# Optimization experiments

Measured on AMD Instinct MI355X. Metric: run time of the kernel, lower is better.

Reference implementation:

```python
import jax, jax.numpy as jnp
import numpy as np


def setup_inputs() -> dict:
    key = jax.random.key(0)
    k1, k2, k3, k4 = jax.random.split(key, 4)
    B, S, D_IN, D_OUT = 32, 4096, 256, 256
    input = jax.random.normal(k1, (B, S, D_IN), dtype=jnp.float32)
    data_mask = jax.random.randint(k2, (B, S), 0, 2).astype(jnp.bool_)
    W = jax.random.normal(k3, (D_IN, D_OUT), dtype=jnp.float32) * (1.0 / np.sqrt(D_IN))
    b = jax.random.normal(k4, (D_OUT,), dtype=jnp.float32) * 0.01
    return {"input": input, "data_mask": data_mask, "W": W, "b": b}


def reference(input, data_mask, W, b):
    # ObjWise: gather non-pad tokens, apply op (Linear+ReLU), scatter back,
    # pad positions filled with zeros. Since the op is per-token, this equals
    # applying the op everywhere and zeroing pad positions.
    # input: (B, S, D_in), data_mask: (B, S)
    y = jax.nn.relu(jnp.einsum("bsd,de->bse", input, W) + b)  # (B, S, D_out)
    return jnp.where(data_mask[..., None], y, jnp.zeros((), dtype=y.dtype))
```

## Files before the change

### kernel.cpp

```cpp
#include <hip/hip_runtime.h>
#include <hip/hip_bf16.h>


typedef __attribute__((ext_vector_type(8))) short bf16x8;
typedef __attribute__((ext_vector_type(4))) float f32x4;
typedef __attribute__((ext_vector_type(2))) unsigned int u32x2;

#define KD 256
#define ND 256
#define BM 64

static __device__ __forceinline__ unsigned short f2bf(float f) {
  union { float f; unsigned u; } x; x.f = f;
  unsigned r = x.u + 0x7FFFu + ((x.u >> 16) & 1u);
  return (unsigned short)(r >> 16);
}

static __device__ __forceinline__ bool mrow(const void* mp, int flag, size_t row) {
  if (flag == 2) return ((const float*)mp)[row] != 0.0f;
  if (flag == 1) return ((const unsigned char*)mp)[row] != 0;
  return ((const int*)mp)[row] != 0;
}

__global__ void prep_w_kernel(const float* __restrict__ W,
                              unsigned short* __restrict__ wf,
                              const unsigned int* __restrict__ mw,
                              int* __restrict__ flag) {
  int k = blockIdx.x;
  int n = threadIdx.x;
  float v = W[k * ND + n];
  int nb = n >> 4;
  int kb = k >> 5;
  int lane = (n & 15) | (((k >> 3) & 3) << 4);
  int e = k & 7;
  wf[(((nb << 3) | kb) << 9) + (lane << 3) + e] = f2bf(v);

  if (blockIdx.x == 0) {
    __shared__ int s;
    if (threadIdx.x == 0) s = 0;
    __syncthreads();
    unsigned w = mw[threadIdx.x];
    int f = 0;
    if (w == 0x3F800000u) f = 2;
    else if (w > 1u) f = 1;
    if (f) atomicOr(&s, f);
    __syncthreads();
    if (threadIdx.x == 0) *flag = (s & 2) ? 2 : (s & 1);
  }
}

__global__ __launch_bounds__(256, 4) void objwise_gemm(
    const float* __restrict__ A, const void* __restrict__ mask,
    const unsigned short* __restrict__ wf, const float* __restrict__ bias,
    float* __restrict__ out, const int* __restrict__ flagp) {
  __shared__ __align__(16) unsigned char As[BM * KD * 2];

  const int flag = *flagp;
  const int tid  = threadIdx.x;
  const int wave = tid >> 6;
  const int lane = tid & 63;
  const size_t rowbase = (size_t)blockIdx.x * BM;

  const float* Ab = A + rowbase * KD;
#pragma unroll
  for (int i = 0; i < 16; ++i) {
    f32x4 v = *(const f32x4*)(Ab + i * 1024 + tid * 4);
    int row  = (i << 2) + (tid >> 6);
    int colb = (tid << 3) & 511;
    int baddr = ((row << 9) | colb) ^ ((row & 7) << 4);
    unsigned p0 = (unsigned)f2bf(v[0]) | ((unsigned)f2bf(v[1]) << 16);
    unsigned p1 = (unsigned)f2bf(v[2]) | ((unsigned)f2bf(v[3]) << 16);
    *(u32x2*)(As + baddr) = (u32x2){p0, p1};
  }
  __syncthreads();

  const int cb = wave << 6;
  const unsigned short* wfl = wf + ((size_t)(cb >> 4) << 12) + (lane << 3);

  f32x4 acc[4][4];
#pragma unroll
  for (int fr = 0; fr < 4; ++fr)
#pragma unroll
    for (int nb = 0; nb < 4; ++nb)
      acc[fr][nb] = (f32x4){0.f, 0.f, 0.f, 0.f};

  const int arow_l = lane & 15;
  const int gbyte  = (lane >> 4) << 4;

#pragma unroll 2
  for (int kb = 0; kb < 8; ++kb) {
    bf16x8 af[4];
#pragma unroll
    for (int fr = 0; fr < 4; ++fr) {
      int row  = (fr << 4) + arow_l;
      int addr = (((row << 9) | ((kb << 6) + gbyte))) ^ ((row & 7) << 4);
      af[fr] = *(const bf16x8*)(As + addr);
    }
#pragma unroll
    for (int nb = 0; nb < 4; ++nb) {
      bf16x8 bfr = *(const bf16x8*)(wfl + ((size_t)nb << 12) + (kb << 9));
      acc[0][nb] = __builtin_amdgcn_mfma_f32_16x16x32_bf16(af[0], bfr, acc[0][nb], 0, 0, 0);
      acc[1][nb] = __builtin_amdgcn_mfma_f32_16x16x32_bf16(af[1], bfr, acc[1][nb], 0, 0, 0);
      acc[2][nb] = __builtin_amdgcn_mfma_f32_16x16x32_bf16(af[2], bfr, acc[2][nb], 0, 0, 0);
      acc[3][nb] = __builtin_amdgcn_mfma_f32_16x16x32_bf16(af[3], bfr, acc[3][nb], 0, 0, 0);
    }
  }

  const int col0 = cb + (lane & 15);
  float bvs[4];
#pragma unroll
  for (int nb = 0; nb < 4; ++nb) bvs[nb] = bias[col0 + (nb << 4)];

#pragma unroll
  for (int fr = 0; fr < 4; ++fr) {
    const int rl = (fr << 4) + ((lane >> 4) << 2);
#pragma unroll
    for (int j = 0; j < 4; ++j) {
      const size_t grow = rowbase + rl + j;
      const bool mm = mrow(mask, flag, grow);
      float* op = out + grow * ND + col0;
#pragma unroll
      for (int nb = 0; nb < 4; ++nb) {
        float v = fmaxf(acc[fr][nb][j] + bvs[nb], 0.f);
        op[nb << 4] = mm ? v : 0.f;
      }
    }
  }
}

extern "C" void kernel_launch(void* const* d_in, const int* in_sizes, int n_in,
                              void* d_out, int out_size, void* d_ws, size_t ws_size,
                              hipStream_t stream) {
  const float* A    = (const float*)d_in[0];
  const void*  mask = d_in[1];
  const float* W    = (const float*)d_in[2];
  const float* bias = (const float*)d_in[3];
  float* out = (float*)d_out;

  int* flag = (int*)d_ws;
  unsigned short* wf = (unsigned short*)((char*)d_ws + 256);

  prep_w_kernel<<<256, 256, 0, stream>>>(W, wf, (const unsigned int*)mask, flag);
  objwise_gemm<<<2048, 256, 0, stream>>>(A, mask, wf, bias, out, flag);
}
```

Baseline: 258.6 us.

## Persist blocks over 4 tiles, prefetch next tile, skip loads of masked rows

Each block now handles four consecutive 64-row tiles. The next tile's fp32 input is loaded into registers while the current tile runs its MFMA loop, and the LDS buffer is double-buffered. A wave ballot over the mask lets the kernel skip global loads for padded rows, which cuts input read traffic by about half, and the mask bits are reused in the epilogue. The risks are extra register pressure from the prefetch registers (launch bounds drop to 2 blocks per CU) and a smaller grid.

```diff
diff --git a/kernel.cpp b/kernel.cpp
--- a/kernel.cpp
+++ b/kernel.cpp
@@ -9,6 +9,8 @@
 #define KD 256
 #define ND 256
 #define BM 64
+#define TILES 4
+#define GRID 512
 
 static __device__ __forceinline__ unsigned short f2bf(float f) {
   union { float f; unsigned u; } x; x.f = f;
@@ -49,82 +51,111 @@
   }
 }
 
-__global__ __launch_bounds__(256, 4) void objwise_gemm(
+__global__ __launch_bounds__(256, 2) void objwise_gemm(
     const float* __restrict__ A, const void* __restrict__ mask,
     const unsigned short* __restrict__ wf, const float* __restrict__ bias,
     float* __restrict__ out, const int* __restrict__ flagp) {
-  __shared__ __align__(16) unsigned char As[BM * KD * 2];
+  __shared__ __align__(16) unsigned char As[2][BM * KD * 2];
 
   const int flag = *flagp;
   const int tid  = threadIdx.x;
   const int wave = tid >> 6;
   const int lane = tid & 63;
-  const size_t rowbase = (size_t)blockIdx.x * BM;
+  const int tile0 = blockIdx.x * TILES;
 
-  const float* Ab = A + rowbase * KD;
-#pragma unroll
-  for (int i = 0; i < 16; ++i) {
-    f32x4 v = *(const f32x4*)(Ab + i * 1024 + tid * 4);
-    int row  = (i << 2) + (tid >> 6);
-    int colb = (tid << 3) & 511;
-    int baddr = ((row << 9) | colb) ^ ((row & 7) << 4);
-    unsigned p0 = (unsigned)f2bf(v[0]) | ((unsigned)f2bf(v[1]) << 16);
-    unsigned p1 = (unsigned)f2bf(v[2]) | ((unsigned)f2bf(v[3]) << 16);
-    *(u32x2*)(As + baddr) = (u32x2){p0, p1};
-  }
-  __syncthreads();
+  const int srowL = tid >> 6;
+  const int colb  = (tid << 3) & 511;
 
   const int cb = wave << 6;
   const unsigned short* wfl = wf + ((size_t)(cb >> 4) << 12) + (lane << 3);
 
-  f32x4 acc[4][4];
-#pragma unroll
-  for (int fr = 0; fr < 4; ++fr)
-#pragma unroll
-    for (int nb = 0; nb < 4; ++nb)
-      acc[fr][nb] = (f32x4){0.f, 0.f, 0.f, 0.f};
-
   const int arow_l = lane & 15;
   const int gbyte  = (lane >> 4) << 4;
-
-#pragma unroll 2
-  for (int kb = 0; kb < 8; ++kb) {
-    bf16x8 af[4];
-#pragma unroll
-    for (int fr = 0; fr < 4; ++fr) {
-      int row  = (fr << 4) + arow_l;
-      int addr = (((row << 9) | ((kb << 6) + gbyte))) ^ ((row & 7) << 4);
-      af[fr] = *(const bf16x8*)(As + addr);
-    }
-#pragma unroll
-    for (int nb = 0; nb < 4; ++nb) {
-      bf16x8 bfr = *(const bf16x8*)(wfl + ((size_t)nb << 12) + (kb << 9));
-      acc[0][nb] = __builtin_amdgcn_mfma_f32_16x16x32_bf16(af[0], bfr, acc[0][nb], 0, 0, 0);
-      acc[1][nb] = __builtin_amdgcn_mfma_f32_16x16x32_bf16(af[1], bfr, acc[1][nb], 0, 0, 0);
-      acc[2][nb] = __builtin_amdgcn_mfma_f32_16x16x32_bf16(af[2], bfr, acc[2][nb], 0, 0, 0);
-      acc[3][nb] = __builtin_amdgcn_mfma_f32_16x16x32_bf16(af[3], bfr, acc[3][nb], 0, 0, 0);
-    }
-  }
-
-  const int col0 = cb + (lane & 15);
+  const int col0   = cb + (lane & 15);
   float bvs[4];
 #pragma unroll
   for (int nb = 0; nb < 4; ++nb) bvs[nb] = bias[col0 + (nb << 4)];
 
+  f32x4 pre[16];
 #pragma unroll
-  for (int fr = 0; fr < 4; ++fr) {
-    const int rl = (fr << 4) + ((lane >> 4) << 2);
+  for (int i = 0; i < 16; ++i) pre[i] = (f32x4){0.f, 0.f, 0.f, 0.f};
+
+  unsigned long long bm = __ballot(mrow(mask, flag, (size_t)tile0 * BM + lane));
+  {
+    const float* Ab = A + (size_t)tile0 * BM * KD;
 #pragma unroll
-    for (int j = 0; j < 4; ++j) {
-      const size_t grow = rowbase + rl + j;
-      const bool mm = mrow(mask, flag, grow);
-      float* op = out + grow * ND + col0;
+    for (int i = 0; i < 16; ++i) {
+      int rowL = (i << 2) + srowL;
+      if ((bm >> rowL) & 1ULL) pre[i] = *(const f32x4*)(Ab + i * 1024 + tid * 4);
+    }
+  }
+
+  for (int t = 0; t < TILES; ++t) {
+    const size_t rowbase = (size_t)(tile0 + t) * BM;
+    unsigned char* Al = As[t & 1];
+
+#pragma unroll
+    for (int i = 0; i < 16; ++i) {
+      int row   = (i << 2) + srowL;
+      int baddr = ((row << 9) | colb) ^ ((row & 7) << 4);
+      unsigned p0 = (unsigned)f2bf(pre[i][0]) | ((unsigned)f2bf(pre[i][1]) << 16);
+      unsigned p1 = (unsigned)f2bf(pre[i][2]) | ((unsigned)f2bf(pre[i][3]) << 16);
+      *(u32x2*)(Al + baddr) = (u32x2){p0, p1};
+    }
+    __syncthreads();
+
+    unsigned long long bm_next = 0;
+    if (t + 1 < TILES) {
+      bm_next = __ballot(mrow(mask, flag, rowbase + BM + lane));
+      const float* Ab = A + (rowbase + BM) * KD;
+#pragma unroll
+      for (int i = 0; i < 16; ++i) {
+        int rowL = (i << 2) + srowL;
+        if ((bm_next >> rowL) & 1ULL) pre[i] = *(const f32x4*)(Ab + i * 1024 + tid * 4);
+      }
+    }
+
+    f32x4 acc[4][4];
+#pragma unroll
+    for (int fr = 0; fr < 4; ++fr)
+#pragma unroll
+      for (int nb = 0; nb < 4; ++nb)
+        acc[fr][nb] = (f32x4){0.f, 0.f, 0.f, 0.f};
+
+#pragma unroll 2
+    for (int kb = 0; kb < 8; ++kb) {
+      bf16x8 af[4];
+#pragma unroll
+      for (int fr = 0; fr < 4; ++fr) {
+        int row  = (fr << 4) + arow_l;
+        int addr = (((row << 9) | ((kb << 6) + gbyte))) ^ ((row & 7) << 4);
+        af[fr] = *(const bf16x8*)(Al + addr);
+      }
 #pragma unroll
       for (int nb = 0; nb < 4; ++nb) {
-        float v = fmaxf(acc[fr][nb][j] + bvs[nb], 0.f);
-        op[nb << 4] = mm ? v : 0.f;
+        bf16x8 bfr = *(const bf16x8*)(wfl + ((size_t)nb << 12) + (kb << 9));
+        acc[0][nb] = __builtin_amdgcn_mfma_f32_16x16x32_bf16(af[0], bfr, acc[0][nb], 0, 0, 0);
+        acc[1][nb] = __builtin_amdgcn_mfma_f32_16x16x32_bf16(af[1], bfr, acc[1][nb], 0, 0, 0);
+        acc[2][nb] = __builtin_amdgcn_mfma_f32_16x16x32_bf16(af[2], bfr, acc[2][nb], 0, 0, 0);
+        acc[3][nb] = __builtin_amdgcn_mfma_f32_16x16x32_bf16(af[3], bfr, acc[3][nb], 0, 0, 0);
       }
     }
+
+#pragma unroll
+    for (int fr = 0; fr < 4; ++fr) {
+      const int rl = (fr << 4) + ((lane >> 4) << 2);
+#pragma unroll
+      for (int j = 0; j < 4; ++j) {
+        const bool mm = (bm >> (rl + j)) & 1ULL;
+        float* op = out + (rowbase + rl + j) * ND + col0;
+#pragma unroll
+        for (int nb = 0; nb < 4; ++nb) {
+          float v = fmaxf(acc[fr][nb][j] + bvs[nb], 0.f);
+          op[nb << 4] = mm ? v : 0.f;
+        }
+      }
+    }
+    bm = bm_next;
   }
 }
 
@@ -141,5 +172,5 @@
   unsigned short* wf = (unsigned short*)((char*)d_ws + 256);
 
   prep_w_kernel<<<256, 256, 0, stream>>>(W, wf, (const unsigned int*)mask, flag);
-  objwise_gemm<<<2048, 256, 0, stream>>>(A, mask, wf, bias, out, flag);
+  objwise_gemm<<<GRID, 256, 0, stream>>>(A, mask, wf, bias, out, flag);
 }
```

Result: no change. 255.0 us (-1.4%).
